# Optimization experiments

Hardware: AMD Instinct MI355X
Metric: run time of the kernel (lower is better)

Reference implementation:

```python
import jax, jax.numpy as jnp
import numpy as np

N = 50000
D = 128
E = 600000

def setup_inputs() -> dict:
    key = jax.random.key(0)
    k1, k2, k3, k4, k5 = jax.random.split(key, 5)
    z1 = jax.random.normal(k1, (N, D), dtype=jnp.float32)
    z2 = jax.random.normal(k2, (N, D), dtype=jnp.float32)
    adj_row = jax.random.randint(k3, (E,), 0, N, dtype=jnp.int32)
    adj_col = jax.random.randint(k4, (E,), 0, N, dtype=jnp.int32)
    adj_val = jax.random.uniform(k5, (E,), dtype=jnp.float32)
    a = jnp.full((N, D), 0.5, dtype=jnp.float32)
    b = jnp.full((N, D), 0.5, dtype=jnp.float32)
    alpha = jnp.float32(0.5)
    return {"z1": z1, "z2": z2, "adj_row": adj_row, "adj_col": adj_col,
            "adj_val": adj_val, "a": a, "b": b, "alpha": alpha}

def reference(z1, z2, adj_row, adj_col, adj_val, a, b, alpha):
    # elementwise gated combine: z_i = a*z1 + b*z2   [N, D]
    z_i = a * z1 + b * z2
    # sparse matmul: z_l[r] = sum_e adj_val[e] * z_i[adj_col[e]] for adj_row[e]==r
    msgs = adj_val[:, None] * z_i[adj_col]          # [E, D]
    z_l = jax.ops.segment_sum(msgs, adj_row, num_segments=N)  # [N, D]
    # residual blend
    return alpha * z_l + (1.0 - alpha) * z_i
```

## Files before the change

### kernel.cpp

```cpp
#include <hip/hip_runtime.h>
#include <hip/hip_fp16.h>

#define DDIM 128
#define NPART 8
#define CAP8MAX 16

__global__ void __launch_bounds__(256) build_kernel(
    const float4* __restrict__ z1, const float4* __restrict__ z2,
    const float4* __restrict__ a,  const float4* __restrict__ b,
    uint2* __restrict__ zi16, int n4,
    const int* __restrict__ rows, const int* __restrict__ cols,
    const float* __restrict__ vals,
    unsigned* __restrict__ slots, int* __restrict__ cnt8,
    int* __restrict__ ohead, int* __restrict__ onext,
    int cap8, int N, int E) {
  const int t = (int)blockIdx.x * (int)blockDim.x + threadIdx.x;
  const int stride = (int)gridDim.x * (int)blockDim.x;

  for (int j = t; j < n4; j += stride) {
    float4 A = a[j], B = b[j], X = z1[j], Y = z2[j];
    __half2 h0 = __floats2half2_rn(A.x * X.x + B.x * Y.x,
                                   A.y * X.y + B.y * Y.y);
    __half2 h1 = __floats2half2_rn(A.z * X.z + B.z * Y.z,
                                   A.w * X.w + B.w * Y.w);
    uint2 pk;
    pk.x = *reinterpret_cast<unsigned*>(&h0);
    pk.y = *reinterpret_cast<unsigned*>(&h1);
    zi16[j] = pk;
  }

  const int p = (int)blockIdx.x & (NPART - 1);
  int* __restrict__ mycnt = cnt8 + (size_t)p * N;
  unsigned* __restrict__ myslots = slots + (size_t)p * N * cap8;
  for (int e0 = t; e0 < E; e0 += 2 * stride) {
    const int e1 = e0 + stride;
    const bool has1 = e1 < E;
    const int   r0 = rows[e0];
    const int   c0 = cols[e0];
    const float v0 = vals[e0];
    const int   r1 = has1 ? rows[e1] : 0;
    const int   c1 = has1 ? cols[e1] : 0;
    const float v1 = has1 ? vals[e1] : 0.f;
    const int j0 = atomicAdd(&mycnt[r0], 1);
    const int j1 = has1 ? atomicAdd(&mycnt[r1], 1) : 0;
    if (j0 < cap8) {
      const unsigned hv = (unsigned)__half_as_ushort(__float2half_rn(v0));
      myslots[(size_t)r0 * cap8 + j0] = (unsigned)c0 | (hv << 16);
    } else {
      onext[e0] = atomicExch(&ohead[r0], e0 + 1);
    }
    if (has1) {
      if (j1 < cap8) {
        const unsigned hv = (unsigned)__half_as_ushort(__float2half_rn(v1));
        myslots[(size_t)r1 * cap8 + j1] = (unsigned)c1 | (hv << 16);
      } else {
        onext[e1] = atomicExch(&ohead[r1], e1 + 1);
      }
    }
  }
}

__global__ void __launch_bounds__(256) reduce_kernel(
    const unsigned* __restrict__ slots, const int* __restrict__ cnt8,
    const int* __restrict__ ohead, const int* __restrict__ onext,
    const int* __restrict__ cols, const float* __restrict__ vals,
    const float* __restrict__ alpha_p,
    const __half2* __restrict__ zi16, float2* __restrict__ out2,
    int cap8, int N) {
  const int r = (int)((blockIdx.x * blockDim.x + threadIdx.x) >> 6);
  const int lane = threadIdx.x & 63;
  if (r >= N) return;
  const float alpha = alpha_p[0];

  const __half2 zr16 = zi16[(size_t)r * (DDIM / 2) + lane];

  int mp[NPART];
  uint4 q[NPART];
  bool over = false;
#pragma unroll
  for (int p = 0; p < NPART; ++p) {
    const int dp = cnt8[(size_t)p * N + r];
    mp[p] = dp < cap8 ? dp : cap8;
    over = over || (dp > cap8);
    q[p] = *(const uint4*)(slots + ((size_t)p * N + r) * cap8);
  }

  float2 a0 = make_float2(0.f, 0.f), a1 = a0, a2 = a0, a3 = a0;
#define EDGE(word, ACC)                                                       \
  {                                                                           \
    const unsigned s_ = (word);                                               \
    const float v_ = __half2float(__ushort_as_half((unsigned short)(s_ >> 16)));\
    const float2 f_ =                                                         \
        __half22float2(zi16[(size_t)(s_ & 0xFFFF) * (DDIM / 2) + lane]);      \
    ACC.x += v_ * f_.x;                                                       \
    ACC.y += v_ * f_.y;                                                       \
  }
#pragma unroll
  for (int p = 0; p < NPART; ++p) {
    const int m = mp[p];
    if (m > 0) EDGE(q[p].x, a0)
    if (m > 1) EDGE(q[p].y, a1)
    if (m > 2) EDGE(q[p].z, a2)
    if (m > 3) EDGE(q[p].w, a3)
    if (m > 4) {
      const unsigned* sp = slots + ((size_t)p * N + r) * cap8;
      for (int j = 4; j < m; ++j) EDGE(sp[j], a0)
    }
  }
  if (over) {
    int e1 = ohead[r];
    while (e1 > 0) {
      const int e = e1 - 1;
      e1 = onext[e];
      const float v = vals[e];
      const float2 f = __half22float2(zi16[(size_t)cols[e] * (DDIM / 2) + lane]);
      a0.x += v * f.x; a0.y += v * f.y;
    }
  }
#undef EDGE

  float2 acc;
  acc.x = (a0.x + a1.x) + (a2.x + a3.x);
  acc.y = (a0.y + a1.y) + (a2.y + a3.y);
  const float2 zr = __half22float2(zr16);
  const float om = 1.0f - alpha;
  float2 o;
  o.x = alpha * acc.x + om * zr.x;
  o.y = alpha * acc.y + om * zr.y;
  out2[(size_t)r * (DDIM / 2) + lane] = o;
}

extern "C" void kernel_launch(void* const* d_in, const int* in_sizes, int n_in,
                              void* d_out, int out_size, void* d_ws, size_t ws_size,
                              hipStream_t stream) {
  const float* z1    = (const float*)d_in[0];
  const float* z2    = (const float*)d_in[1];
  const int*   rows  = (const int*)  d_in[2];
  const int*   cols  = (const int*)  d_in[3];
  const float* vals  = (const float*)d_in[4];
  const float* a     = (const float*)d_in[5];
  const float* b     = (const float*)d_in[6];
  const float* alpha = (const float*)d_in[7];
  float* out = (float*)d_out;

  const int ND = in_sizes[0];
  const int E  = in_sizes[2];
  const int N  = ND / DDIM;
  const int n4 = ND / 4;

  __half2* zi16 = (__half2*)d_ws;
  int* cnt8  = (int*)((char*)d_ws + (size_t)ND * 2);
  int* ohead = cnt8 + (size_t)NPART * N;
  int* onext = ohead + N;
  unsigned* slots = (unsigned*)(onext + E);

  const size_t fixed_bytes = (size_t)ND * 2 +
                             ((size_t)NPART * N + N + E) * 4;
  size_t avail = ws_size > fixed_bytes ? ws_size - fixed_bytes : 0;
  int cap8 = (int)(avail / ((size_t)NPART * N * sizeof(unsigned)));
  if (cap8 > CAP8MAX) cap8 = CAP8MAX;
  cap8 &= ~3;
  if (cap8 < 4) cap8 = 0;

  hipMemsetAsync(cnt8, 0x00, (size_t)(NPART + 1) * N * sizeof(int), stream);

  build_kernel<<<2048, 256, 0, stream>>>(
      (const float4*)z1, (const float4*)z2, (const float4*)a,
      (const float4*)b, (uint2*)zi16, n4,
      rows, cols, vals, slots, cnt8, ohead, onext, cap8, N, E);

  const int blocks2 = (int)(((long long)N * 64 + 255) / 256);
  reduce_kernel<<<blocks2, 256, 0, stream>>>(
      slots, cnt8, ohead, onext, cols, vals, alpha,
      zi16, (float2*)out, cap8, N);
}
```

Before: 227.2 us.

## Replace per-partition counters with CAS-probed per-row slot table

Drops the 8-way partitioned counter arrays. Each edge is now inserted into a single 32-entry per-row slot array, starting at a hash of the edge index and using linear probing with atomicCAS on an empty sentinel. The reduce kernel reads all 32 slots unconditionally and skips empty ones, which removes the counter reads and the per-partition bounds logic. In exchange, the slot array must be memset to 0xFF, CAS probing can retry several times, and every row now reads 128 bytes of slots regardless of its degree. Column indices are packed into 16 bits and 0xFFFF marks an empty slot, so this only holds for N under 65535.

```diff
diff --git a/kernel.cpp b/kernel.cpp
--- a/kernel.cpp
+++ b/kernel.cpp
@@ -2,8 +2,8 @@
 #include <hip/hip_fp16.h>
 
 #define DDIM 128
-#define NPART 8
-#define CAP8MAX 16
+#define CAP 32
+#define EMPTYW 0xFFFFFFFFu
 
 __global__ void __launch_bounds__(256) build_kernel(
     const float4* __restrict__ z1, const float4* __restrict__ z2,
@@ -11,9 +11,8 @@
     uint2* __restrict__ zi16, int n4,
     const int* __restrict__ rows, const int* __restrict__ cols,
     const float* __restrict__ vals,
-    unsigned* __restrict__ slots, int* __restrict__ cnt8,
-    int* __restrict__ ohead, int* __restrict__ onext,
-    int cap8, int N, int E) {
+    unsigned* __restrict__ slots,
+    int* __restrict__ ohead, int* __restrict__ onext, int E) {
   const int t = (int)blockIdx.x * (int)blockDim.x + threadIdx.x;
   const int stride = (int)gridDim.x * (int)blockDim.x;
 
@@ -29,44 +28,31 @@
     zi16[j] = pk;
   }
 
-  const int p = (int)blockIdx.x & (NPART - 1);
-  int* __restrict__ mycnt = cnt8 + (size_t)p * N;
-  unsigned* __restrict__ myslots = slots + (size_t)p * N * cap8;
-  for (int e0 = t; e0 < E; e0 += 2 * stride) {
-    const int e1 = e0 + stride;
-    const bool has1 = e1 < E;
-    const int   r0 = rows[e0];
-    const int   c0 = cols[e0];
-    const float v0 = vals[e0];
-    const int   r1 = has1 ? rows[e1] : 0;
-    const int   c1 = has1 ? cols[e1] : 0;
-    const float v1 = has1 ? vals[e1] : 0.f;
-    const int j0 = atomicAdd(&mycnt[r0], 1);
-    const int j1 = has1 ? atomicAdd(&mycnt[r1], 1) : 0;
-    if (j0 < cap8) {
-      const unsigned hv = (unsigned)__half_as_ushort(__float2half_rn(v0));
-      myslots[(size_t)r0 * cap8 + j0] = (unsigned)c0 | (hv << 16);
-    } else {
-      onext[e0] = atomicExch(&ohead[r0], e0 + 1);
+  for (int e = t; e < E; e += stride) {
+    const int   r = rows[e];
+    const int   c = cols[e];
+    const float v = vals[e];
+    const unsigned hv = (unsigned)__half_as_ushort(__float2half_rn(v));
+    const unsigned pk = (unsigned)c | (hv << 16);
+    unsigned* __restrict__ rowp = slots + (size_t)r * CAP;
+    int h = e & (CAP - 1);
+    bool done = false;
+    for (int tr = 0; tr < CAP; ++tr) {
+      const unsigned old = atomicCAS(&rowp[h], EMPTYW, pk);
+      if (old == EMPTYW) { done = true; break; }
+      h = (h + 1) & (CAP - 1);
     }
-    if (has1) {
-      if (j1 < cap8) {
-        const unsigned hv = (unsigned)__half_as_ushort(__float2half_rn(v1));
-        myslots[(size_t)r1 * cap8 + j1] = (unsigned)c1 | (hv << 16);
-      } else {
-        onext[e1] = atomicExch(&ohead[r1], e1 + 1);
-      }
-    }
+    if (!done)
+      onext[e] = atomicExch(&ohead[r], e + 1);
   }
 }
 
 __global__ void __launch_bounds__(256) reduce_kernel(
-    const unsigned* __restrict__ slots, const int* __restrict__ cnt8,
+    const unsigned* __restrict__ slots,
     const int* __restrict__ ohead, const int* __restrict__ onext,
     const int* __restrict__ cols, const float* __restrict__ vals,
     const float* __restrict__ alpha_p,
-    const __half2* __restrict__ zi16, float2* __restrict__ out2,
-    int cap8, int N) {
+    const __half2* __restrict__ zi16, float2* __restrict__ out2, int N) {
   const int r = (int)((blockIdx.x * blockDim.x + threadIdx.x) >> 6);
   const int lane = threadIdx.x & 63;
   if (r >= N) return;
@@ -74,50 +60,46 @@
 
   const __half2 zr16 = zi16[(size_t)r * (DDIM / 2) + lane];
 
-  int mp[NPART];
-  uint4 q[NPART];
-  bool over = false;
+  const uint4* sp4 = (const uint4*)(slots + (size_t)r * CAP);
+  uint4 q[CAP / 4];
 #pragma unroll
-  for (int p = 0; p < NPART; ++p) {
-    const int dp = cnt8[(size_t)p * N + r];
-    mp[p] = dp < cap8 ? dp : cap8;
-    over = over || (dp > cap8);
-    q[p] = *(const uint4*)(slots + ((size_t)p * N + r) * cap8);
-  }
+  for (int p = 0; p < CAP / 4; ++p) q[p] = sp4[p];
 
   float2 a0 = make_float2(0.f, 0.f), a1 = a0, a2 = a0, a3 = a0;
-#define EDGE(word, ACC)                                                       \
-  {                                                                           \
-    const unsigned s_ = (word);                                               \
-    const float v_ = __half2float(__ushort_as_half((unsigned short)(s_ >> 16)));\
-    const float2 f_ =                                                         \
-        __half22float2(zi16[(size_t)(s_ & 0xFFFF) * (DDIM / 2) + lane]);      \
-    ACC.x += v_ * f_.x;                                                       \
-    ACC.y += v_ * f_.y;                                                       \
+  bool full = true;
+#define EDGE(word, ACC)                                                        \
+  {                                                                            \
+    const unsigned s_ = (word);                                                \
+    if ((s_ & 0xFFFFu) != 0xFFFFu) {                                           \
+      const float v_ =                                                         \
+          __half2float(__ushort_as_half((unsigned short)(s_ >> 16)));          \
+      const float2 f_ =                                                        \
+          __half22float2(zi16[(size_t)(s_ & 0xFFFFu) * (DDIM / 2) + lane]);    \
+      ACC.x += v_ * f_.x;                                                      \
+      ACC.y += v_ * f_.y;                                                      \
+    } else {                                                                   \
+      full = false;                                                            \
+    }                                                                          \
   }
 #pragma unroll
-  for (int p = 0; p < NPART; ++p) {
-    const int m = mp[p];
-    if (m > 0) EDGE(q[p].x, a0)
-    if (m > 1) EDGE(q[p].y, a1)
-    if (m > 2) EDGE(q[p].z, a2)
-    if (m > 3) EDGE(q[p].w, a3)
-    if (m > 4) {
-      const unsigned* sp = slots + ((size_t)p * N + r) * cap8;
-      for (int j = 4; j < m; ++j) EDGE(sp[j], a0)
-    }
+  for (int p = 0; p < CAP / 4; ++p) {
+    EDGE(q[p].x, a0)
+    EDGE(q[p].y, a1)
+    EDGE(q[p].z, a2)
+    EDGE(q[p].w, a3)
   }
-  if (over) {
+#undef EDGE
+  if (full) {
     int e1 = ohead[r];
     while (e1 > 0) {
       const int e = e1 - 1;
       e1 = onext[e];
       const float v = vals[e];
-      const float2 f = __half22float2(zi16[(size_t)cols[e] * (DDIM / 2) + lane]);
+      const float2 f =
+          __half22float2(zi16[(size_t)cols[e] * (DDIM / 2) + lane]);
       a0.x += v * f.x; a0.y += v * f.y;
     }
   }
-#undef EDGE
 
   float2 acc;
   acc.x = (a0.x + a1.x) + (a2.x + a3.x);
@@ -149,28 +131,20 @@
   const int n4 = ND / 4;
 
   __half2* zi16 = (__half2*)d_ws;
-  int* cnt8  = (int*)((char*)d_ws + (size_t)ND * 2);
-  int* ohead = cnt8 + (size_t)NPART * N;
+  int* ohead = (int*)((char*)d_ws + (size_t)ND * 2);
   int* onext = ohead + N;
   unsigned* slots = (unsigned*)(onext + E);
 
-  const size_t fixed_bytes = (size_t)ND * 2 +
-                             ((size_t)NPART * N + N + E) * 4;
-  size_t avail = ws_size > fixed_bytes ? ws_size - fixed_bytes : 0;
-  int cap8 = (int)(avail / ((size_t)NPART * N * sizeof(unsigned)));
-  if (cap8 > CAP8MAX) cap8 = CAP8MAX;
-  cap8 &= ~3;
-  if (cap8 < 4) cap8 = 0;
-
-  hipMemsetAsync(cnt8, 0x00, (size_t)(NPART + 1) * N * sizeof(int), stream);
+  hipMemsetAsync(ohead, 0x00, (size_t)N * sizeof(int), stream);
+  hipMemsetAsync(slots, 0xFF, (size_t)N * CAP * sizeof(unsigned), stream);
 
   build_kernel<<<2048, 256, 0, stream>>>(
       (const float4*)z1, (const float4*)z2, (const float4*)a,
       (const float4*)b, (uint2*)zi16, n4,
-      rows, cols, vals, slots, cnt8, ohead, onext, cap8, N, E);
+      rows, cols, vals, slots, ohead, onext, E);
 
   const int blocks2 = (int)(((long long)N * 64 + 255) / 256);
   reduce_kernel<<<blocks2, 256, 0, stream>>>(
-      slots, cnt8, ohead, onext, cols, vals, alpha,
-      zi16, (float2*)out, cap8, N);
+      slots, ohead, onext, cols, vals, alpha,
+      zi16, (float2*)out, N);
 }
```

Measured after the change: 215.2 us. -5.3%, faster.
